# Performance work log

Hardware: AMD Instinct MI355X
Metric: run time of the kernel (lower is better)

## Reference

```python
import jax, jax.numpy as jnp
import numpy as np

EPS = 1e-6
DROP_RATE = 0.25

def setup_inputs() -> dict:
    key = jax.random.key(0)
    k1, k2, k3 = jax.random.split(key, 3)
    B, S, D = 4, 2048, 2048
    inputs = jax.random.normal(k1, (B, S, D), dtype=jnp.float32)
    # keras 'uniform' initializer: U(-0.05, 0.05)
    W_1 = jax.random.uniform(k2, (D, D), dtype=jnp.float32, minval=-0.05, maxval=0.05)
    W_2 = jax.random.uniform(k3, (D, D), dtype=jnp.float32, minval=-0.05, maxval=0.05)
    return {"inputs": inputs, "W_1": W_1, "W_2": W_2}

def reference(inputs, W_1, W_2):
    # LayerNorm over last axis (no affine: gamma/beta unused in original call)
    mean = jnp.mean(inputs, axis=-1, keepdims=True)
    var = jnp.mean(jnp.square(inputs - mean), axis=-1, keepdims=True)
    x_norm = (inputs - mean) / jnp.sqrt(var + EPS)          # [B,S,D]
    # 2-layer MLP with relu
    h = jax.nn.relu(jnp.einsum('bsd,de->bse', x_norm, W_1))  # [B,S,D]
    y = jnp.einsum('bsd,de->bse', h, W_2)                    # [B,S,D]
    # dropout(0.25), inverted scaling, fixed key for determinism
    keep = jax.random.bernoulli(jax.random.key(1), 1.0 - DROP_RATE, y.shape)
    y_drop = jnp.where(keep, y / (1.0 - DROP_RATE), 0.0)
    return x_norm + y_drop
```

## Files before the change

kernel.cpp:

```cpp
#include <hip/hip_runtime.h>
#include <hip/hip_bf16.h>
#include <stdint.h>

#define M_DIM 8192
#define N_DIM 2048
#define K_DIM 2048

typedef __bf16 bf16x8_t __attribute__((ext_vector_type(8)));
typedef float f32x4_t __attribute__((ext_vector_type(4)));

__device__ __forceinline__ unsigned tf_rotl(unsigned x, int r) {
  return (x << r) | (x >> (32 - r));
}
__device__ __forceinline__ unsigned threefry_mask_bits(unsigned ctr) {
  unsigned x0 = 0u, x1 = ctr;
  const unsigned ks0 = 0u, ks1 = 1u, ks2 = 0x1BD11BDBu;
  x0 += ks0; x1 += ks1;
#define TFR(r) { x0 += x1; x1 = tf_rotl(x1, (r)); x1 ^= x0; }
  TFR(13) TFR(15) TFR(26) TFR(6)
  x0 += ks1; x1 += ks2 + 1u;
  TFR(17) TFR(29) TFR(16) TFR(24)
  x0 += ks2; x1 += ks0 + 2u;
  TFR(13) TFR(15) TFR(26) TFR(6)
  x0 += ks0; x1 += ks1 + 3u;
  TFR(17) TFR(29) TFR(16) TFR(24)
  x0 += ks1; x1 += ks2 + 4u;
  TFR(13) TFR(15) TFR(26) TFR(6)
  x0 += ks2; x1 += ks0 + 5u;
#undef TFR
  return x0 ^ x1;
}

__device__ __forceinline__ void gload_lds16(const __hip_bfloat16* g, unsigned short* l) {
  __builtin_amdgcn_global_load_lds(
      (const __attribute__((address_space(1))) unsigned int*)g,
      (__attribute__((address_space(3))) unsigned int*)l,
      16, 0, 0);
}

__global__ __launch_bounds__(256) void wt_kernel(
    const float* __restrict__ W1, const float* __restrict__ W2,
    __hip_bfloat16* __restrict__ W1t, __hip_bfloat16* __restrict__ W2t) {
  __shared__ float tile[32][33];
  const float* src = blockIdx.z ? W2 : W1;
  __hip_bfloat16* dst = blockIdx.z ? W2t : W1t;
  int x = blockIdx.x * 32 + threadIdx.x;
  int y = blockIdx.y * 32 + threadIdx.y;
#pragma unroll
  for (int i = 0; i < 32; i += 8)
    tile[threadIdx.y + i][threadIdx.x] = src[(size_t)(y + i) * N_DIM + x];
  __syncthreads();
  int xo = blockIdx.y * 32 + threadIdx.x;
  int yo = blockIdx.x * 32 + threadIdx.y;
#pragma unroll
  for (int i = 0; i < 32; i += 8)
    dst[(size_t)(yo + i) * K_DIM + xo] = __float2bfloat16(tile[threadIdx.x][threadIdx.y + i]);
}

__global__ __launch_bounds__(256) void ln_kernel(const float* __restrict__ X,
                                                 __hip_bfloat16* __restrict__ Xn) {
  const int row = blockIdx.x;
  const float4* xv = (const float4*)(X + (size_t)row * K_DIM);
  float4 v0 = xv[threadIdx.x];
  float4 v1 = xv[threadIdx.x + 256];
  float s  = v0.x + v0.y + v0.z + v0.w + v1.x + v1.y + v1.z + v1.w;
  float ss = v0.x*v0.x + v0.y*v0.y + v0.z*v0.z + v0.w*v0.w
           + v1.x*v1.x + v1.y*v1.y + v1.z*v1.z + v1.w*v1.w;
#pragma unroll
  for (int off = 32; off > 0; off >>= 1) {
    s  += __shfl_xor(s, off);
    ss += __shfl_xor(ss, off);
  }
  __shared__ float rs[4], rss[4];
  const int wave = threadIdx.x >> 6;
  if ((threadIdx.x & 63) == 0) { rs[wave] = s; rss[wave] = ss; }
  __syncthreads();
  float S  = rs[0] + rs[1] + rs[2] + rs[3];
  float SS = rss[0] + rss[1] + rss[2] + rss[3];
  float mean = S * (1.0f / 2048.0f);
  float var  = SS * (1.0f / 2048.0f) - mean * mean;
  float rstd = 1.0f / sqrtf(var + 1e-6f);
  float vv[8] = {v0.x, v0.y, v0.z, v0.w, v1.x, v1.y, v1.z, v1.w};
  unsigned short o[8];
#pragma unroll
  for (int i = 0; i < 8; i++) {
    __hip_bfloat16 b = __float2bfloat16((vv[i] - mean) * rstd);
    o[i] = *(unsigned short*)&b;
  }
  ushort4* dst = (ushort4*)(Xn + (size_t)row * K_DIM);
  dst[threadIdx.x]       = make_ushort4(o[0], o[1], o[2], o[3]);
  dst[threadIdx.x + 256] = make_ushort4(o[4], o[5], o[6], o[7]);
}

template <int EPI>
__global__ __launch_bounds__(512, 2) void gemm256(
    const __hip_bfloat16* __restrict__ A,
    const __hip_bfloat16* __restrict__ Bt,
    const __hip_bfloat16* __restrict__ Xn,
    __hip_bfloat16* __restrict__ Hout,
    float* __restrict__ Fout) {
  __shared__ unsigned short As[2][16384];
  __shared__ unsigned short Bs[2][16384];
  const int tid  = threadIdx.x;
  const int lane = tid & 63;
  const int wave = tid >> 6;
  const int wm = wave >> 2;
  const int wn = wave & 3;

  const int bid = blockIdx.x;
  const int wg  = (bid & 7) * 32 + (bid >> 3);
  const int mBase = (wg & 31) << 8;
  const int nBase = (wg >> 5) << 8;

  f32x4_t acc[8][4];
#pragma unroll
  for (int i = 0; i < 8; i++)
#pragma unroll
    for (int j = 0; j < 4; j++) acc[i][j] = (f32x4_t){0.f, 0.f, 0.f, 0.f};

  const int rowIn = lane >> 3;
  const int csrc  = ((lane & 7) ^ (rowIn & 7)) << 3;
  const __hip_bfloat16* aSrcB = A  + (size_t)(mBase + 8 * wave + rowIn) * K_DIM + csrc;
  const int bRowW = ((wave >> 2) << 6) + ((wave & 3) << 3);
  const __hip_bfloat16* bSrcB = Bt + (size_t)(nBase + bRowW + rowIn) * K_DIM + csrc;
  const int aDst = wave << 9;
  const int bDst = bRowW << 6;

#define STA(b, h, k)                                                                         \
  gload_lds16(aSrcB + (size_t)((h) * 64) * K_DIM + (k), &As[b][aDst + (h) * 4096]);          \
  gload_lds16(aSrcB + (size_t)((h) * 64 + 128) * K_DIM + (k), &As[b][aDst + (h) * 4096 + 8192]);
#define STB(b, h, k)                                                                         \
  gload_lds16(bSrcB + (size_t)((h) * 32) * K_DIM + (k), &Bs[b][bDst + (h) * 2048]);          \
  gload_lds16(bSrcB + (size_t)((h) * 32 + 128) * K_DIM + (k), &Bs[b][bDst + (h) * 2048 + 8192]);

  const int fr = lane & 15;
  const int fq = lane >> 4;
  const int c0 = ((fq)     ^ (fr & 7)) << 3;
  const int c1 = ((4 | fq) ^ (fr & 7)) << 3;
  const int aRd = (wm * 128 + fr) * 64;
  const int bRd = (wn * 64  + fr) * 64;

  bf16x8_t aF[4][2], bF[4][2];
#define RDA(b, f)                                                      \
  aF[(f) & 3][0] = *(const bf16x8_t*)&As[b][aRd + (f) * 1024 + c0];    \
  aF[(f) & 3][1] = *(const bf16x8_t*)&As[b][aRd + (f) * 1024 + c1];
#define RDB(b, nf)                                                     \
  bF[nf][0] = *(const bf16x8_t*)&Bs[b][bRd + (nf) * 1024 + c0];        \
  bF[nf][1] = *(const bf16x8_t*)&Bs[b][bRd + (nf) * 1024 + c1];

#define MFMAQ(mh, nlo)                                                             \
  _Pragma("unroll")                                                                \
  for (int mi = 0; mi < 4; mi++) {                                                 \
    _Pragma("unroll")                                                              \
    for (int nj = 0; nj < 2; nj++) {                                               \
      acc[(mh) * 4 + mi][(nlo) + nj] = __builtin_amdgcn_mfma_f32_16x16x32_bf16(    \
          aF[mi][0], bF[(nlo) + nj][0], acc[(mh) * 4 + mi][(nlo) + nj], 0, 0, 0);  \
      acc[(mh) * 4 + mi][(nlo) + nj] = __builtin_amdgcn_mfma_f32_16x16x32_bf16(    \
          aF[mi][1], bF[(nlo) + nj][1], acc[(mh) * 4 + mi][(nlo) + nj], 0, 0, 0);  \
    }                                                                              \
  }

#define BAR() __builtin_amdgcn_s_barrier()
#define LGKM0()                                              \
  {                                                          \
    asm volatile("s_waitcnt lgkmcnt(0)" ::: "memory");       \
    __builtin_amdgcn_sched_barrier(0);                       \
  }
#define LGKM8() asm volatile("s_waitcnt lgkmcnt(8)" ::: "memory")
#define VMW(n)                                               \
  {                                                          \
    asm volatile("s_waitcnt vmcnt(" #n ")" ::: "memory");    \
    __builtin_amdgcn_sched_barrier(0);                       \
  }

#define TILE(t, S1, S2, S3, S4, VMODE)                                   \
  {                                                                      \
    const int buf = (t) & 1;                                             \
     \
    RDA(buf, 0) RDA(buf, 1) RDA(buf, 2) RDA(buf, 3)                      \
    RDB(buf, 0) RDB(buf, 1)                                              \
    if (S1) { STB(buf ^ 1, 1, ((t) + 1) * 64) }                          \
    LGKM8(); BAR(); LGKM0();                                             \
    __builtin_amdgcn_s_setprio(1); MFMAQ(0, 0)                           \
    __builtin_amdgcn_s_setprio(0); BAR();                                \
     \
    RDB(buf, 2) RDB(buf, 3)                                              \
    if (S2) { STA(buf, 0, ((t) + 2) * 64) }                              \
    BAR(); LGKM0();                                                      \
    __builtin_amdgcn_s_setprio(1); MFMAQ(0, 2)                           \
    __builtin_amdgcn_s_setprio(0); BAR();                                \
     \
    RDA(buf, 4) RDA(buf, 5) RDA(buf, 6) RDA(buf, 7)                      \
    if (S3) { STB(buf, 0, ((t) + 2) * 64) }                              \
    BAR(); LGKM0();                                                      \
    __builtin_amdgcn_s_setprio(1); MFMAQ(1, 0)                           \
    __builtin_amdgcn_s_setprio(0); BAR();                                \
    \
    if (S4) { STA(buf, 1, ((t) + 2) * 64) }                              \
    if ((VMODE) == 0) { VMW(6); } else if ((VMODE) == 1) { VMW(0); }     \
    BAR();                                                               \
    __builtin_amdgcn_s_setprio(1); MFMAQ(1, 2)                           \
    __builtin_amdgcn_s_setprio(0); BAR();                                \
  }

  STA(0, 0, 0) STB(0, 0, 0) STA(0, 1, 0) STB(0, 1, 0)
  VMW(4);
  STA(1, 0, 64) STB(1, 0, 64) STA(1, 1, 64)
  VMW(6);
  BAR();

  for (int t = 0; t < 30; ++t) {
    TILE(t, 1, 1, 1, 1, 0)
  }
  TILE(30, 1, 0, 0, 0, 1)
  TILE(31, 0, 0, 0, 0, 2)

#undef TILE
#undef STA
#undef STB
#undef RDA
#undef RDB
#undef MFMAQ
#undef BAR
#undef LGKM0
#undef LGKM8
#undef VMW

  const int mW = mBase + wm * 128 + fq * 4;
  const int nW = nBase + wn * 64 + fr;
#pragma unroll
  for (int f = 0; f < 8; f++) {
#pragma unroll
    for (int nf = 0; nf < 4; nf++) {
      const int n  = nW + nf * 16;
      const int m0 = mW + f * 16;
#pragma unroll
      for (int r = 0; r < 4; r++) {
        float v = acc[f][nf][r];
        size_t j = (size_t)(m0 + r) * N_DIM + n;
        if (EPI == 0) {
          Hout[j] = __float2bfloat16(fmaxf(v, 0.0f));
        } else {
          unsigned bits = threefry_mask_bits((unsigned)j);
          float y  = (bits < 0xC0000000u) ? v * (1.0f / 0.75f) : 0.0f;
          Fout[j]  = __bfloat162float(Xn[j]) + y;
        }
      }
    }
  }
}

extern "C" void kernel_launch(void* const* d_in, const int* in_sizes, int n_in,
                              void* d_out, int out_size, void* d_ws, size_t ws_size,
                              hipStream_t stream) {
  (void)in_sizes; (void)n_in; (void)out_size; (void)ws_size;
  const float* X  = (const float*)d_in[0];
  const float* W1 = (const float*)d_in[1];
  const float* W2 = (const float*)d_in[2];
  float* out = (float*)d_out;

  unsigned char* ws = (unsigned char*)d_ws;
  __hip_bfloat16* Xn  = (__hip_bfloat16*)(ws);
  __hip_bfloat16* H   = (__hip_bfloat16*)(ws + ((size_t)32 << 20));
  __hip_bfloat16* W1t = (__hip_bfloat16*)(ws + ((size_t)64 << 20));
  __hip_bfloat16* W2t = (__hip_bfloat16*)(ws + ((size_t)72 << 20));

  wt_kernel<<<dim3(64, 64, 2), dim3(32, 8, 1), 0, stream>>>(W1, W2, W1t, W2t);
  ln_kernel<<<M_DIM, 256, 0, stream>>>(X, Xn);
  gemm256<0><<<dim3(256, 1, 1), dim3(512, 1, 1), 0, stream>>>(Xn, W1t, nullptr, H, nullptr);
  gemm256<1><<<dim3(256, 1, 1), dim3(512, 1, 1), 0, stream>>>(H, W2t, Xn, nullptr, out);
}
```

Before: 342.5 us.

## Restructure GEMM main loop into k-half phases with reordered LDS prefetch

Reorganizes each K-tile into four phases split by k-half (ck0/ck1) and M-half, so each phase loads 4 A fragments and reuses 4 B fragments across a full 4x4 MFMA block instead of 2-wide n chunks. It also reorders the global-to-LDS prefetch schedule (B for the next tile plus half of A issued early, the other A half two tiles ahead), manually unrolls by two so buffer indices are compile-time constants, and relaxes the vmcnt wait. The aim is lower fragment register pressure and better overlap of loads with MFMA, with more LGKM waits per tile as the trade-off.

```diff
diff --git a/kernel.cpp b/kernel.cpp
--- a/kernel.cpp
+++ b/kernel.cpp
@@ -135,28 +135,33 @@
 
   const int fr = lane & 15;
   const int fq = lane >> 4;
-  const int c0 = ((fq)     ^ (fr & 7)) << 3;
-  const int c1 = ((4 | fq) ^ (fr & 7)) << 3;
+  const int ck0 = ((fq)     ^ (fr & 7)) << 3;
+  const int ck1 = ((4 | fq) ^ (fr & 7)) << 3;
   const int aRd = (wm * 128 + fr) * 64;
   const int bRd = (wn * 64  + fr) * 64;
 
-  bf16x8_t aF[4][2], bF[4][2];
-#define RDA(b, f)                                                      \
-  aF[(f) & 3][0] = *(const bf16x8_t*)&As[b][aRd + (f) * 1024 + c0];    \
-  aF[(f) & 3][1] = *(const bf16x8_t*)&As[b][aRd + (f) * 1024 + c1];
-#define RDB(b, nf)                                                     \
-  bF[nf][0] = *(const bf16x8_t*)&Bs[b][bRd + (nf) * 1024 + c0];        \
-  bF[nf][1] = *(const bf16x8_t*)&Bs[b][bRd + (nf) * 1024 + c1];
-
-#define MFMAQ(mh, nlo)                                                             \
+  bf16x8_t aF[4];
+  bf16x8_t bK0[4];
+  bf16x8_t bK1[4];
+
+#define RDA4(B, MH, CK)                                                       \
+  aF[0] = *(const bf16x8_t*)&As[B][aRd + (MH) * 4096 + 0 * 1024 + (CK)];      \
+  aF[1] = *(const bf16x8_t*)&As[B][aRd + (MH) * 4096 + 1 * 1024 + (CK)];      \
+  aF[2] = *(const bf16x8_t*)&As[B][aRd + (MH) * 4096 + 2 * 1024 + (CK)];      \
+  aF[3] = *(const bf16x8_t*)&As[B][aRd + (MH) * 4096 + 3 * 1024 + (CK)];
+#define RDB4(B, DST, CK)                                                      \
+  DST[0] = *(const bf16x8_t*)&Bs[B][bRd + 0 * 1024 + (CK)];                   \
+  DST[1] = *(const bf16x8_t*)&Bs[B][bRd + 1 * 1024 + (CK)];                   \
+  DST[2] = *(const bf16x8_t*)&Bs[B][bRd + 2 * 1024 + (CK)];                   \
+  DST[3] = *(const bf16x8_t*)&Bs[B][bRd + 3 * 1024 + (CK)];
+
+#define MFMAP(MH, BARR)                                                            \
   _Pragma("unroll")                                                                \
   for (int mi = 0; mi < 4; mi++) {                                                 \
     _Pragma("unroll")                                                              \
-    for (int nj = 0; nj < 2; nj++) {                                               \
-      acc[(mh) * 4 + mi][(nlo) + nj] = __builtin_amdgcn_mfma_f32_16x16x32_bf16(    \
-          aF[mi][0], bF[(nlo) + nj][0], acc[(mh) * 4 + mi][(nlo) + nj], 0, 0, 0);  \
-      acc[(mh) * 4 + mi][(nlo) + nj] = __builtin_amdgcn_mfma_f32_16x16x32_bf16(    \
-          aF[mi][1], bF[(nlo) + nj][1], acc[(mh) * 4 + mi][(nlo) + nj], 0, 0, 0);  \
+    for (int nf = 0; nf < 4; nf++) {                                               \
+      acc[(MH) * 4 + mi][nf] = __builtin_amdgcn_mfma_f32_16x16x32_bf16(            \
+          aF[mi], BARR[nf], acc[(MH) * 4 + mi][nf], 0, 0, 0);                      \
     }                                                                              \
   }
 
@@ -166,64 +171,62 @@
     asm volatile("s_waitcnt lgkmcnt(0)" ::: "memory");       \
     __builtin_amdgcn_sched_barrier(0);                       \
   }
-#define LGKM8() asm volatile("s_waitcnt lgkmcnt(8)" ::: "memory")
 #define VMW(n)                                               \
   {                                                          \
     asm volatile("s_waitcnt vmcnt(" #n ")" ::: "memory");    \
     __builtin_amdgcn_sched_barrier(0);                       \
   }
 
-#define TILE(t, S1, S2, S3, S4, VMODE)                                   \
+#define TILE(T, BUF, OBUF, S1, S3, VMODE)                                \
   {                                                                      \
-    const int buf = (t) & 1;                                             \
-     \
-    RDA(buf, 0) RDA(buf, 1) RDA(buf, 2) RDA(buf, 3)                      \
-    RDB(buf, 0) RDB(buf, 1)                                              \
-    if (S1) { STB(buf ^ 1, 1, ((t) + 1) * 64) }                          \
-    LGKM8(); BAR(); LGKM0();                                             \
-    __builtin_amdgcn_s_setprio(1); MFMAQ(0, 0)                           \
-    __builtin_amdgcn_s_setprio(0); BAR();                                \
-     \
-    RDB(buf, 2) RDB(buf, 3)                                              \
-    if (S2) { STA(buf, 0, ((t) + 2) * 64) }                              \
-    BAR(); LGKM0();                                                      \
-    __builtin_amdgcn_s_setprio(1); MFMAQ(0, 2)                           \
-    __builtin_amdgcn_s_setprio(0); BAR();                                \
-     \
-    RDA(buf, 4) RDA(buf, 5) RDA(buf, 6) RDA(buf, 7)                      \
-    if (S3) { STB(buf, 0, ((t) + 2) * 64) }                              \
-    BAR(); LGKM0();                                                      \
-    __builtin_amdgcn_s_setprio(1); MFMAQ(1, 0)                           \
-    __builtin_amdgcn_s_setprio(0); BAR();                                \
-    \
-    if (S4) { STA(buf, 1, ((t) + 2) * 64) }                              \
-    if ((VMODE) == 0) { VMW(6); } else if ((VMODE) == 1) { VMW(0); }     \
-    BAR();                                                               \
-    __builtin_amdgcn_s_setprio(1); MFMAQ(1, 2)                           \
-    __builtin_amdgcn_s_setprio(0); BAR();                                \
-  }
-
-  STA(0, 0, 0) STB(0, 0, 0) STA(0, 1, 0) STB(0, 1, 0)
-  VMW(4);
-  STA(1, 0, 64) STB(1, 0, 64) STA(1, 1, 64)
-  VMW(6);
+       \
+    RDA4(BUF, 0, ck0) RDB4(BUF, bK0, ck0)                                \
+    if (S1) {                                                            \
+      STB(OBUF, 0, ((T) + 1) * 64) STB(OBUF, 1, ((T) + 1) * 64)          \
+      STA(OBUF, 1, ((T) + 1) * 64)                                       \
+    }                                                                    \
+    BAR(); LGKM0();                                                      \
+    __builtin_amdgcn_s_setprio(1); MFMAP(0, bK0)                         \
+    __builtin_amdgcn_s_setprio(0); BAR();                                \
+                                                       \
+    RDA4(BUF, 0, ck1) RDB4(BUF, bK1, ck1)                                \
+    BAR(); LGKM0();                                                      \
+    __builtin_amdgcn_s_setprio(1); MFMAP(0, bK1)                         \
+    __builtin_amdgcn_s_setprio(0); BAR();                                \
+       \
+    RDA4(BUF, 1, ck0)                                                    \
+    if (S3) { STA(BUF, 0, ((T) + 2) * 64) }                              \
+    BAR(); LGKM0();                                                      \
+    __builtin_amdgcn_s_setprio(1); MFMAP(1, bK0)                         \
+    __builtin_amdgcn_s_setprio(0); BAR();                                \
+                            \
+    RDA4(BUF, 1, ck1)                                                    \
+    if ((VMODE) == 0) { VMW(2); } else if ((VMODE) == 1) { VMW(0); }     \
+    BAR(); LGKM0();                                                      \
+    __builtin_amdgcn_s_setprio(1); MFMAP(1, bK1)                         \
+    __builtin_amdgcn_s_setprio(0); BAR();                                \
+  }
+
+  STA(0, 0, 0) STA(0, 1, 0) STB(0, 0, 0) STB(0, 1, 0)
+  STA(1, 0, 64)
+  VMW(2);
   BAR();
 
-  for (int t = 0; t < 30; ++t) {
-    TILE(t, 1, 1, 1, 1, 0)
-  }
-  TILE(30, 1, 0, 0, 0, 1)
-  TILE(31, 0, 0, 0, 0, 2)
+  for (int t = 0; t < 30; t += 2) {
+    TILE(t,     0, 1, 1, 1, 0)
+    TILE(t + 1, 1, 0, 1, 1, 0)
+  }
+  TILE(30, 0, 1, 1, 0, 1)
+  TILE(31, 1, 0, 0, 0, 2)
 
 #undef TILE
 #undef STA
 #undef STB
-#undef RDA
-#undef RDB
-#undef MFMAQ
+#undef RDA4
+#undef RDB4
+#undef MFMAP
 #undef BAR
 #undef LGKM0
-#undef LGKM8
 #undef VMW
 
   const int mW = mBase + wm * 128 + fq * 4;
```

New measurement: 342.1 us. No clear change (-0.1%).
